# Optimization experiments

Measured on AMD Instinct MI355X. Metric: run time of the kernel, lower is better.

## Reference

```python
import jax, jax.numpy as jnp
import numpy as np

N = 8192
D = 512


def setup_inputs() -> dict:
    key = jax.random.key(0)
    k1, k2, k3, k4 = jax.random.split(key, 4)
    U = jax.random.normal(k1, (N, D), dtype=jnp.float32)
    V = jax.random.normal(k2, (N, D), dtype=jnp.float32)
    M = jax.random.normal(k3, (N, N), dtype=jnp.float32)
    W = jax.random.uniform(k4, (N, N), dtype=jnp.float32)
    alpha = jnp.ones((1,), dtype=jnp.float32) * 0.1
    return {"U": U, "V": V, "M": M, "W": W, "alpha": alpha}


def reference(U, V, M, W, alpha):
    # Reconstruction term: sum((U V^T - M)^2)
    recon = U @ V.T                                  # (N, N) GEMM
    part1 = jnp.sum(jnp.square(recon - M))
    # Manifold term in closed form:
    # sum_{i,j} W[i,j] * ||U_i - V_j||^2
    #   = sum_i rowW_i ||U_i||^2 + sum_j colW_j ||V_j||^2 - 2 sum(W * U V^T)
    u_sq = jnp.sum(U * U, axis=1)                    # (N,)
    v_sq = jnp.sum(V * V, axis=1)                    # (N,)
    row_w = jnp.sum(W, axis=1)                       # (N,)
    col_w = jnp.sum(W, axis=0)                       # (N,)
    cross = jnp.sum(W * recon)
    part2 = alpha[0] * (jnp.dot(row_w, u_sq) + jnp.dot(col_w, v_sq) - 2.0 * cross)
    total = part1 + part2
    return total / (M.shape[0] * M.shape[1])
```

## Files before the change

kernel.cpp:

```cpp
#include <hip/hip_runtime.h>
#include <hip/hip_bf16.h>
#include <stdint.h>

#define N_DIM 8192
#define D_DIM 512
#define BM 128
#define BN 128
#define BK 64
#define RSTR 136
#define TPB 4

typedef __attribute__((ext_vector_type(8))) short bf16x8;
typedef __attribute__((ext_vector_type(4))) float f32x4;

__device__ __forceinline__ unsigned short f2bf(float f) {
    unsigned int x = __float_as_uint(f);
    x += 0x7fffu + ((x >> 16) & 1u);
    return (unsigned short)(x >> 16);
}
__device__ __forceinline__ float bf2f(unsigned short u) {
    return __uint_as_float(((unsigned int)u) << 16);
}

__global__ void __launch_bounds__(256) prep_kernel(
    const float* __restrict__ U, const float* __restrict__ V,
    unsigned short* __restrict__ Ub, unsigned short* __restrict__ Vb,
    float* __restrict__ usq, float* __restrict__ vsq)
{
    int row = blockIdx.x;
    const float* src;
    unsigned short* dst;
    float* sq;
    if (row < N_DIM) {
        src = U + (size_t)row * D_DIM;
        dst = Ub + (size_t)row * D_DIM;
        sq  = usq + row;
    } else {
        int r = row - N_DIM;
        src = V + (size_t)r * D_DIM;
        dst = Vb + (size_t)r * D_DIM;
        sq  = vsq + r;
    }
    int t = threadIdx.x;
    float2 v = *reinterpret_cast<const float2*>(src + 2 * t);
    float s = v.x * v.x + v.y * v.y;
    ushort2 b;
    b.x = f2bf(v.x);
    b.y = f2bf(v.y);
    *reinterpret_cast<ushort2*>(dst + 2 * t) = b;

    #pragma unroll
    for (int o = 32; o > 0; o >>= 1) s += __shfl_down(s, o, 64);
    __shared__ float red[4];
    if ((t & 63) == 0) red[t >> 6] = s;
    __syncthreads();
    if (t == 0) *sq = red[0] + red[1] + red[2] + red[3];
}

__global__ void __launch_bounds__(256, 2) fused_kernel(
    const unsigned short* __restrict__ Ub, const unsigned short* __restrict__ Vb,
    const float* __restrict__ Mg, const float* __restrict__ Wg,
    const float* __restrict__ usq, const float* __restrict__ vsq,
    double* __restrict__ acc)
{
    __shared__ alignas(16) char smem[BM * BK * 2 + BN * BK * 2];
    __shared__ alignas(16) unsigned short recs[BM * RSTR];
    __shared__ float red1[4], red2[4];
    char* As = smem;
    char* Bs = smem + BM * BK * 2;

    const int t    = threadIdx.x;
    const int lane = t & 63;
    const int wave = t >> 6;
    const int wm   = wave >> 1;
    const int wn   = wave & 1;

    const int bid    = blockIdx.x;
    const int tile_m = bid >> 4;
    const int quad   = bid & 15;
    const int row0   = tile_m * BM;

    const int rg = t >> 4;
    const int ct = t & 15;
    const int c8 = ct * 8;

    float s1 = 0.f, s2 = 0.f;

    auto As3 = (__attribute__((address_space(3))) char*)As;
    auto Bs3 = (__attribute__((address_space(3))) char*)Bs;

    auto stage = [&](const unsigned short* Ua, const unsigned short* Va, int k0) {
        #pragma unroll
        for (int c = 0; c < 4; ++c) {
            int s   = c * 256 + t;
            int row = s >> 3;
            int kg  = s & 7;
            int kgs = kg ^ (row & 7);
            __builtin_amdgcn_global_load_lds(
                (const __attribute__((address_space(1))) void*)(Ua + (size_t)row * D_DIM + k0 + kgs * 8),
                (__attribute__((address_space(3))) void*)(As3 + s * 16), 16, 0, 0);
            __builtin_amdgcn_global_load_lds(
                (const __attribute__((address_space(1))) void*)(Va + (size_t)row * D_DIM + k0 + kgs * 8),
                (__attribute__((address_space(3))) void*)(Bs3 + s * 16), 16, 0, 0);
        }
    };

    auto mma = [&](f32x4 (&a)[4][4]) {
        #pragma unroll
        for (int kc = 0; kc < 2; ++kc) {
            bf16x8 af[4], bfr[4];
            const int kgw = kc * 4 + (lane >> 4);
            #pragma unroll
            for (int i = 0; i < 4; ++i) {
                int ra = wm * 64 + i * 16 + (lane & 15);
                af[i]  = *reinterpret_cast<const bf16x8*>(As + ra * (BK * 2) + ((kgw ^ (ra & 7)) * 16));
                int rb = wn * 64 + i * 16 + (lane & 15);
                bfr[i] = *reinterpret_cast<const bf16x8*>(Bs + rb * (BK * 2) + ((kgw ^ (rb & 7)) * 16));
            }
            #pragma unroll
            for (int i = 0; i < 4; ++i)
                #pragma unroll
                for (int j = 0; j < 4; ++j)
                    a[i][j] = __builtin_amdgcn_mfma_f32_16x16x32_bf16(af[i], bfr[j], a[i][j], 0, 0, 0);
        }
    };

    auto dump = [&](f32x4 (&a)[4][4]) {
        #pragma unroll
        for (int i = 0; i < 4; ++i)
            #pragma unroll
            for (int j = 0; j < 4; ++j)
                #pragma unroll
                for (int q = 0; q < 4; ++q) {
                    int r = wm * 64 + i * 16 + (lane >> 4) * 4 + q;
                    int c = wn * 64 + j * 16 + (lane & 15);
                    recs[r * RSTR + c] = f2bf(a[i][j][q]);
                }
    };

    int   colp = 0;
    f32x4 vs0v, vs1v;

    auto issue = [&](int chunk, f32x4& m0, f32x4& m1, f32x4& w0, f32x4& w1, float& us) {
        int r = chunk * 16 + rg;
        const float* Mp = Mg + (size_t)(row0 + r) * N_DIM + colp + c8;
        const float* Wp = Wg + (size_t)(row0 + r) * N_DIM + colp + c8;
        m0 = *reinterpret_cast<const f32x4*>(Mp);
        m1 = *reinterpret_cast<const f32x4*>(Mp + 4);
        w0 = *reinterpret_cast<const f32x4*>(Wp);
        w1 = *reinterpret_cast<const f32x4*>(Wp + 4);
        us = usq[row0 + r];
    };

    auto consume = [&](int chunk, f32x4 m0, f32x4 m1, f32x4 w0, f32x4 w1, float us) {
        int r = chunk * 16 + rg;
        bf16x8 rb = *reinterpret_cast<const bf16x8*>(&recs[r * RSTR + c8]);
        #pragma unroll
        for (int c = 0; c < 4; ++c) {
            float rc = bf2f((unsigned short)rb[c]);
            float d  = rc - m0[c];
            s1 = fmaf(d, d, s1);
            s2 = fmaf(w0[c], us + vs0v[c] - 2.f * rc, s2);
        }
        #pragma unroll
        for (int c = 0; c < 4; ++c) {
            float rc = bf2f((unsigned short)rb[4 + c]);
            float d  = rc - m1[c];
            s1 = fmaf(d, d, s1);
            s2 = fmaf(w1[c], us + vs1v[c] - 2.f * rc, s2);
        }
    };

    const f32x4 zero = {0.f, 0.f, 0.f, 0.f};
    const unsigned short* Ua = Ub + (size_t)row0 * D_DIM;

    f32x4 a[4][4];
    f32x4 mvA[2], wvA[2], mvB[2], wvB[2];
    float usA, usB;

    for (int it = 0; it < TPB; ++it) {
        const int col0 = (quad * TPB + it) * BN;
        const unsigned short* Va = Vb + (size_t)col0 * D_DIM;
        const bool strm = (it > 0);

        #pragma unroll
        for (int i = 0; i < 4; ++i)
            #pragma unroll
            for (int j = 0; j < 4; ++j) a[i][j] = zero;

        if (strm) {
            colp = (quad * TPB + it - 1) * BN;
            vs0v = *reinterpret_cast<const f32x4*>(vsq + colp + c8);
            vs1v = *reinterpret_cast<const f32x4*>(vsq + colp + c8 + 4);
            issue(0, mvA[0], mvA[1], wvA[0], wvA[1], usA);
        }

        #pragma unroll
        for (int kt = 0; kt < D_DIM / BK; ++kt) {
            stage(Ua, Va, kt * BK);
            __syncthreads();
            if (strm && kt < 7) {
                if (kt & 1) issue(kt + 1, mvA[0], mvA[1], wvA[0], wvA[1], usA);
                else        issue(kt + 1, mvB[0], mvB[1], wvB[0], wvB[1], usB);
            }
            mma(a);
            if (strm) {
                if (kt & 1) consume(kt, mvB[0], mvB[1], wvB[0], wvB[1], usB);
                else        consume(kt, mvA[0], mvA[1], wvA[0], wvA[1], usA);
            }
            __syncthreads();
        }
        dump(a);
    }

    colp = (quad * TPB + TPB - 1) * BN;
    vs0v = *reinterpret_cast<const f32x4*>(vsq + colp + c8);
    vs1v = *reinterpret_cast<const f32x4*>(vsq + colp + c8 + 4);
    __syncthreads();
    issue(0, mvA[0], mvA[1], wvA[0], wvA[1], usA);
    #pragma unroll
    for (int chunk = 0; chunk < 8; ++chunk) {
        if (chunk < 7) {
            if (chunk & 1) issue(chunk + 1, mvA[0], mvA[1], wvA[0], wvA[1], usA);
            else           issue(chunk + 1, mvB[0], mvB[1], wvB[0], wvB[1], usB);
        }
        if (chunk & 1) consume(chunk, mvB[0], mvB[1], wvB[0], wvB[1], usB);
        else           consume(chunk, mvA[0], mvA[1], wvA[0], wvA[1], usA);
    }

    #pragma unroll
    for (int o = 32; o > 0; o >>= 1) {
        s1 += __shfl_down(s1, o, 64);
        s2 += __shfl_down(s2, o, 64);
    }
    if (lane == 0) { red1[wave] = s1; red2[wave] = s2; }
    __syncthreads();
    if (t == 0) {
        double a1s = (double)red1[0] + red1[1] + red1[2] + red1[3];
        double a2s = (double)red2[0] + red2[1] + red2[2] + red2[3];
        atomicAdd(acc, a1s);
        atomicAdd(acc + 1, a2s);
    }
}

__global__ void finalize_kernel(const double* __restrict__ acc,
                                const float* __restrict__ alpha,
                                float* __restrict__ out)
{
    double tot = acc[0] + (double)alpha[0] * acc[1];
    out[0] = (float)(tot / ((double)N_DIM * (double)N_DIM));
}

extern "C" void kernel_launch(void* const* d_in, const int* in_sizes, int n_in,
                              void* d_out, int out_size, void* d_ws, size_t ws_size,
                              hipStream_t stream) {
    const float* U     = (const float*)d_in[0];
    const float* V     = (const float*)d_in[1];
    const float* Mg    = (const float*)d_in[2];
    const float* Wg    = (const float*)d_in[3];
    const float* alpha = (const float*)d_in[4];

    char* ws = (char*)d_ws;
    unsigned short* Ub = (unsigned short*)ws;
    unsigned short* Vb = (unsigned short*)(ws + 8u * 1024 * 1024);
    float* usq = (float*)(ws + 16u * 1024 * 1024);
    float* vsq = (float*)(ws + 16u * 1024 * 1024 + 32u * 1024);
    double* acc = (double*)(ws + 16u * 1024 * 1024 + 64u * 1024);

    hipMemsetAsync(acc, 0, 2 * sizeof(double), stream);
    prep_kernel<<<2 * N_DIM, 256, 0, stream>>>(U, V, Ub, Vb, usq, vsq);
    fused_kernel<<<(N_DIM / BM) * (N_DIM / BN) / TPB, 256, 0, stream>>>(
        Ub, Vb, Mg, Wg, usq, vsq, acc);
    finalize_kernel<<<1, 1, 0, stream>>>(acc, alpha, (float*)d_out);
}
```

Baseline: 218.7 us.

## Replace global_load_lds staging with register-staged LDS writes and manual barriers

Operand tiles now load from global memory into registers and are then written to swizzled LDS, replacing the direct global-to-LDS loads. Barriers use an explicit lgkmcnt(0) wait plus s_barrier, so the wait covers only LDS traffic and the outstanding M/W global prefetches can stay in flight across the barrier. The K loop is unrolled by two with dedicated A/B register sets, and the recon buffer stride changes from 136 to 140. The intent is to overlap the streaming M/W reads with the MFMA work more effectively. In exchange it uses more registers, which may lower occupancy, and the hand-written waitcnt and barrier ordering is fragile.

After: 178.7 us. 18.3% less time.

```diff
diff --git a/kernel.cpp b/kernel.cpp
--- a/kernel.cpp
+++ b/kernel.cpp
@@ -7,11 +7,12 @@
 #define BM 128
 #define BN 128
 #define BK 64
-#define RSTR 136
+#define RSTR 140
 #define TPB 4
 
 typedef __attribute__((ext_vector_type(8))) short bf16x8;
 typedef __attribute__((ext_vector_type(4))) float f32x4;
+typedef __attribute__((ext_vector_type(4))) unsigned int u32x4;
 
 __device__ __forceinline__ unsigned short f2bf(float f) {
     unsigned int x = __float_as_uint(f);
@@ -81,27 +82,92 @@
     const int row0   = tile_m * BM;
 
     const int rg = t >> 4;
-    const int ct = t & 15;
-    const int c8 = ct * 8;
+    const int c8 = (t & 15) * 8;
 
     float s1 = 0.f, s2 = 0.f;
 
-    auto As3 = (__attribute__((address_space(3))) char*)As;
-    auto Bs3 = (__attribute__((address_space(3))) char*)Bs;
-
-    auto stage = [&](const unsigned short* Ua, const unsigned short* Va, int k0) {
+    int   colp = 0;
+    f32x4 vs0, vs1;
+    f32x4 mA0, mA1, wA0, wA1; float usA;
+    f32x4 mB0, mB1, wB0, wB1; float usB;
+
+    auto issueA = [&](int chunk) {
+        int r = chunk * 16 + rg;
+        const float* Mp = Mg + (size_t)(row0 + r) * N_DIM + colp + c8;
+        const float* Wp = Wg + (size_t)(row0 + r) * N_DIM + colp + c8;
+        mA0 = *reinterpret_cast<const f32x4*>(Mp);
+        mA1 = *reinterpret_cast<const f32x4*>(Mp + 4);
+        wA0 = *reinterpret_cast<const f32x4*>(Wp);
+        wA1 = *reinterpret_cast<const f32x4*>(Wp + 4);
+        usA = usq[row0 + r];
+    };
+    auto issueB = [&](int chunk) {
+        int r = chunk * 16 + rg;
+        const float* Mp = Mg + (size_t)(row0 + r) * N_DIM + colp + c8;
+        const float* Wp = Wg + (size_t)(row0 + r) * N_DIM + colp + c8;
+        mB0 = *reinterpret_cast<const f32x4*>(Mp);
+        mB1 = *reinterpret_cast<const f32x4*>(Mp + 4);
+        wB0 = *reinterpret_cast<const f32x4*>(Wp);
+        wB1 = *reinterpret_cast<const f32x4*>(Wp + 4);
+        usB = usq[row0 + r];
+    };
+    auto consumeA = [&](int chunk) {
+        int r = chunk * 16 + rg;
+        bf16x8 rb = *reinterpret_cast<const bf16x8*>(&recs[r * RSTR + c8]);
+        #pragma unroll
+        for (int c = 0; c < 4; ++c) {
+            float rc = bf2f((unsigned short)rb[c]);
+            float d  = rc - mA0[c];
+            s1 = fmaf(d, d, s1);
+            s2 = fmaf(wA0[c], usA + vs0[c] - 2.f * rc, s2);
+        }
+        #pragma unroll
+        for (int c = 0; c < 4; ++c) {
+            float rc = bf2f((unsigned short)rb[4 + c]);
+            float d  = rc - mA1[c];
+            s1 = fmaf(d, d, s1);
+            s2 = fmaf(wA1[c], usA + vs1[c] - 2.f * rc, s2);
+        }
+    };
+    auto consumeB = [&](int chunk) {
+        int r = chunk * 16 + rg;
+        bf16x8 rb = *reinterpret_cast<const bf16x8*>(&recs[r * RSTR + c8]);
+        #pragma unroll
+        for (int c = 0; c < 4; ++c) {
+            float rc = bf2f((unsigned short)rb[c]);
+            float d  = rc - mB0[c];
+            s1 = fmaf(d, d, s1);
+            s2 = fmaf(wB0[c], usB + vs0[c] - 2.f * rc, s2);
+        }
+        #pragma unroll
+        for (int c = 0; c < 4; ++c) {
+            float rc = bf2f((unsigned short)rb[4 + c]);
+            float d  = rc - mB1[c];
+            s1 = fmaf(d, d, s1);
+            s2 = fmaf(wB1[c], usB + vs1[c] - 2.f * rc, s2);
+        }
+    };
+
+    auto stage_load = [&](const unsigned short* Ua, const unsigned short* Va, int k0,
+                          u32x4 (&sa)[4], u32x4 (&sb)[4]) {
+        #pragma unroll
+        for (int c = 0; c < 4; ++c) {
+            int s   = c * 256 + t;
+            int row = s >> 3;
+            int kg  = s & 7;
+            sa[c] = *reinterpret_cast<const u32x4*>(Ua + (size_t)row * D_DIM + k0 + kg * 8);
+            sb[c] = *reinterpret_cast<const u32x4*>(Va + (size_t)row * D_DIM + k0 + kg * 8);
+        }
+    };
+    auto stage_write = [&](u32x4 (&sa)[4], u32x4 (&sb)[4]) {
         #pragma unroll
         for (int c = 0; c < 4; ++c) {
             int s   = c * 256 + t;
             int row = s >> 3;
             int kg  = s & 7;
             int kgs = kg ^ (row & 7);
-            __builtin_amdgcn_global_load_lds(
-                (const __attribute__((address_space(1))) void*)(Ua + (size_t)row * D_DIM + k0 + kgs * 8),
-                (__attribute__((address_space(3))) void*)(As3 + s * 16), 16, 0, 0);
-            __builtin_amdgcn_global_load_lds(
-                (const __attribute__((address_space(1))) void*)(Va + (size_t)row * D_DIM + k0 + kgs * 8),
-                (__attribute__((address_space(3))) void*)(Bs3 + s * 16), 16, 0, 0);
+            *reinterpret_cast<u32x4*>(As + row * (BK * 2) + kgs * 16) = sa[c];
+            *reinterpret_cast<u32x4*>(Bs + row * (BK * 2) + kgs * 16) = sb[c];
         }
     };
 
@@ -138,45 +204,15 @@
                 }
     };
 
-    int   colp = 0;
-    f32x4 vs0v, vs1v;
-
-    auto issue = [&](int chunk, f32x4& m0, f32x4& m1, f32x4& w0, f32x4& w1, float& us) {
-        int r = chunk * 16 + rg;
-        const float* Mp = Mg + (size_t)(row0 + r) * N_DIM + colp + c8;
-        const float* Wp = Wg + (size_t)(row0 + r) * N_DIM + colp + c8;
-        m0 = *reinterpret_cast<const f32x4*>(Mp);
-        m1 = *reinterpret_cast<const f32x4*>(Mp + 4);
-        w0 = *reinterpret_cast<const f32x4*>(Wp);
-        w1 = *reinterpret_cast<const f32x4*>(Wp + 4);
-        us = usq[row0 + r];
-    };
-
-    auto consume = [&](int chunk, f32x4 m0, f32x4 m1, f32x4 w0, f32x4 w1, float us) {
-        int r = chunk * 16 + rg;
-        bf16x8 rb = *reinterpret_cast<const bf16x8*>(&recs[r * RSTR + c8]);
-        #pragma unroll
-        for (int c = 0; c < 4; ++c) {
-            float rc = bf2f((unsigned short)rb[c]);
-            float d  = rc - m0[c];
-            s1 = fmaf(d, d, s1);
-            s2 = fmaf(w0[c], us + vs0v[c] - 2.f * rc, s2);
-        }
-        #pragma unroll
-        for (int c = 0; c < 4; ++c) {
-            float rc = bf2f((unsigned short)rb[4 + c]);
-            float d  = rc - m1[c];
-            s1 = fmaf(d, d, s1);
-            s2 = fmaf(w1[c], us + vs1v[c] - 2.f * rc, s2);
-        }
-    };
-
     const f32x4 zero = {0.f, 0.f, 0.f, 0.f};
     const unsigned short* Ua = Ub + (size_t)row0 * D_DIM;
-
     f32x4 a[4][4];
-    f32x4 mvA[2], wvA[2], mvB[2], wvB[2];
-    float usA, usB;
+    u32x4 sa[4], sb[4];
+
+    #define FENCE() asm volatile("" ::: "memory")
+    #define LGKM0_BAR() do { \
+        asm volatile("s_waitcnt lgkmcnt(0)" ::: "memory"); \
+        __builtin_amdgcn_s_barrier(); } while (0)
 
     for (int it = 0; it < TPB; ++it) {
         const int col0 = (quad * TPB + it) * BN;
@@ -189,44 +225,51 @@
             for (int j = 0; j < 4; ++j) a[i][j] = zero;
 
         if (strm) {
-            colp = (quad * TPB + it - 1) * BN;
-            vs0v = *reinterpret_cast<const f32x4*>(vsq + colp + c8);
-            vs1v = *reinterpret_cast<const f32x4*>(vsq + colp + c8 + 4);
-            issue(0, mvA[0], mvA[1], wvA[0], wvA[1], usA);
-        }
-
-        #pragma unroll
-        for (int kt = 0; kt < D_DIM / BK; ++kt) {
-            stage(Ua, Va, kt * BK);
-            __syncthreads();
-            if (strm && kt < 7) {
-                if (kt & 1) issue(kt + 1, mvA[0], mvA[1], wvA[0], wvA[1], usA);
-                else        issue(kt + 1, mvB[0], mvB[1], wvB[0], wvB[1], usB);
-            }
+            colp = col0 - BN;
+            vs0 = *reinterpret_cast<const f32x4*>(vsq + colp + c8);
+            vs1 = *reinterpret_cast<const f32x4*>(vsq + colp + c8 + 4);
+            issueA(0);
+        }
+
+        for (int kt2 = 0; kt2 < 4; ++kt2) {
+            const int kt = kt2 * 2;
+            stage_load(Ua, Va, kt * BK, sa, sb);
+            FENCE();
+            if (strm) issueB(kt + 1);
+            FENCE();
+            stage_write(sa, sb);
+            LGKM0_BAR();
             mma(a);
-            if (strm) {
-                if (kt & 1) consume(kt, mvB[0], mvB[1], wvB[0], wvB[1], usB);
-                else        consume(kt, mvA[0], mvA[1], wvA[0], wvA[1], usA);
-            }
-            __syncthreads();
+            if (strm) consumeA(kt);
+            LGKM0_BAR();
+
+            stage_load(Ua, Va, (kt + 1) * BK, sa, sb);
+            FENCE();
+            if (strm && kt2 < 3) issueA(kt + 2);
+            FENCE();
+            stage_write(sa, sb);
+            LGKM0_BAR();
+            mma(a);
+            if (strm) consumeB(kt + 1);
+            LGKM0_BAR();
         }
         dump(a);
     }
 
     colp = (quad * TPB + TPB - 1) * BN;
-    vs0v = *reinterpret_cast<const f32x4*>(vsq + colp + c8);
-    vs1v = *reinterpret_cast<const f32x4*>(vsq + colp + c8 + 4);
-    __syncthreads();
-    issue(0, mvA[0], mvA[1], wvA[0], wvA[1], usA);
-    #pragma unroll
-    for (int chunk = 0; chunk < 8; ++chunk) {
-        if (chunk < 7) {
-            if (chunk & 1) issue(chunk + 1, mvA[0], mvA[1], wvA[0], wvA[1], usA);
-            else           issue(chunk + 1, mvB[0], mvB[1], wvB[0], wvB[1], usB);
-        }
-        if (chunk & 1) consume(chunk, mvB[0], mvB[1], wvB[0], wvB[1], usB);
-        else           consume(chunk, mvA[0], mvA[1], wvA[0], wvA[1], usA);
-    }
+    vs0 = *reinterpret_cast<const f32x4*>(vsq + colp + c8);
+    vs1 = *reinterpret_cast<const f32x4*>(vsq + colp + c8 + 4);
+    LGKM0_BAR();
+    issueA(0);
+    issueB(1);
+    consumeA(0); issueA(2);
+    consumeB(1); issueB(3);
+    consumeA(2); issueA(4);
+    consumeB(3); issueB(5);
+    consumeA(4); issueA(6);
+    consumeB(5); issueB(7);
+    consumeA(6);
+    consumeB(7);
 
     #pragma unroll
     for (int o = 32; o > 0; o >>= 1) {
@@ -241,6 +284,8 @@
         atomicAdd(acc, a1s);
         atomicAdd(acc + 1, a2s);
     }
+    #undef FENCE
+    #undef LGKM0_BAR
 }
 
 __global__ void finalize_kernel(const double* __restrict__ acc,
```
